# Kernel tuning notes

Hardware: AMD Instinct MI355X
Metric: run time of the kernel (lower is better)

The kernel has to match this reference:

```python
import jax, jax.numpy as jnp
import numpy as np

C = 1024      # num_classes (leaves of a balanced binary tree)
E = 10        # num_edges = tree depth (log2(C))
B = 8192      # batch size


def _build_hierarchy_buffers():
    """Replicates HierarchicalLLLoss.__init__ for a balanced binary tree.

    edges_from_leaf[i][j] is leaf i's ancestor edge j levels up (j=0 is the
    leaf's own edge). Its leaf set is all leaves sharing the top (E-j) bits,
    i.e. l >> j == i >> j.
    """
    i = np.arange(C)
    onehot_num = np.zeros((C, C, E), dtype=np.float32)
    onehot_den = np.zeros((C, C, E), dtype=np.float32)
    for j in range(E):
        onehot_num[:, :, j] = ((i[:, None] >> j) == (i[None, :] >> j))
    for j in range(E - 1):
        # den column j uses the ancestor one level higher (edges_from_leaf[i][1:])
        onehot_den[:, :, j] = ((i[:, None] >> (j + 1)) == (i[None, :] >> (j + 1)))
    onehot_den[:, :, E - 1] = 1.0  # root: all leaves
    # per-edge weights: exponential decay with level (leaf edge heaviest)
    w = np.exp(-0.5 * np.arange(E, dtype=np.float32))
    weights = np.broadcast_to(w, (C, E)).copy()
    return (jnp.asarray(onehot_num), jnp.asarray(onehot_den), jnp.asarray(weights))


def setup_inputs() -> dict:
    key = jax.random.key(0)
    k1, k2 = jax.random.split(key)
    # inputs are softmax-style probabilities (strictly positive)
    logits = jax.random.uniform(k1, (B, C), dtype=jnp.float32, minval=0.0, maxval=1.0)
    inputs = logits / jnp.sum(logits, axis=1, keepdims=True)
    target = jax.random.randint(k2, (B,), 0, C, dtype=jnp.int64 if jax.config.read('jax_enable_x64') else jnp.int32)
    onehot_num, onehot_den, weights = _build_hierarchy_buffers()
    return {"inputs": inputs, "target": target,
            "onehot_num": onehot_num, "onehot_den": onehot_den,
            "weights": weights}


def reference(inputs, target, onehot_num, onehot_den, weights):
    # gather per-sample onehot slabs: [B, C, E]
    oh_num = onehot_num[target]
    oh_den = onehot_den[target]
    # bmm(inputs[B,1,C], oh[B,C,E]) -> [B, E]
    num = jnp.einsum('bc,bce->be', inputs, oh_num)
    den = jnp.einsum('bc,bce->be', inputs, oh_den)
    idx = num != 0
    safe_num = jnp.where(idx, num, 1.0)
    safe_den = jnp.where(idx, den, 1.0)
    terms = jnp.where(idx, -jnp.log(safe_num / safe_den), num)
    per_sample = jnp.sum(jnp.flip(weights[target] * terms, axis=1), axis=1)
    return jnp.mean(per_sample)
```

## Files before the change

### kernel.cpp

```cpp
#include <hip/hip_runtime.h>

#define C_CLASSES 1024
#define E_EDGES   10
#define BATCH     8192
#define WPB       4
#define NBLOCKS   (BATCH / WPB)

__device__ __constant__ const float WLN2[E_EDGES] = {
    0.69314718f, 0.42041501f, 0.25499462f, 0.15466204f, 0.09380727f,
    0.05689699f, 0.03450977f, 0.02093123f, 0.01269543f, 0.00770017f};

__global__ __launch_bounds__(256) void hll_main(const float* __restrict__ in,
                                                const int*   __restrict__ tgt,
                                                float* __restrict__ loss) {
    const int tid  = threadIdx.x;
    const int lane = tid & 63;
    const int wave = tid >> 6;
    const int b    = blockIdx.x * WPB + wave;

    const int t = tgt[b];
    const float* row = in + (size_t)b * C_CLASSES + lane * 16;
    const float4 a0 = ((const float4*)row)[0];
    const float4 a1 = ((const float4*)row)[1];
    const float4 a2 = ((const float4*)row)[2];
    const float4 a3 = ((const float4*)row)[3];

    const float p0 = a0.x + a0.y, p1 = a0.z + a0.w;
    const float p2 = a1.x + a1.y, p3 = a1.z + a1.w;
    const float p4 = a2.x + a2.y, p5 = a2.z + a2.w;
    const float p6 = a3.x + a3.y, p7 = a3.z + a3.w;
    const float q0 = p0 + p1, q1 = p2 + p3;
    const float q2 = p4 + p5, q3 = p6 + p7;
    const float r0 = q0 + q1, r1 = q2 + q3;
    float T = r0 + r1;

    const float s4 = T;
    T += __shfl_xor(T, 1);  const float s5  = T;
    T += __shfl_xor(T, 2);  const float s6  = T;
    T += __shfl_xor(T, 4);  const float s7  = T;
    T += __shfl_xor(T, 8);  const float s8  = T;
    T += __shfl_xor(T, 16); const float s9  = T;
    T += __shfl_xor(T, 32); const float s10 = T;

    if (lane == (t >> 4)) {
        const int ti = t & 15;
        const float s3 = (ti & 8) ? r1 : r0;
        const float s2 = (ti & 8) ? ((ti & 4) ? q3 : q2)
                                  : ((ti & 4) ? q1 : q0);
        const float s1 = (ti & 8) ? ((ti & 4) ? ((ti & 2) ? p7 : p6)
                                              : ((ti & 2) ? p5 : p4))
                                  : ((ti & 4) ? ((ti & 2) ? p3 : p2)
                                              : ((ti & 2) ? p1 : p0));
        const float s0 =
            (ti & 8) ? ((ti & 4) ? ((ti & 2) ? ((ti & 1) ? a3.w : a3.z)
                                             : ((ti & 1) ? a3.y : a3.x))
                                 : ((ti & 2) ? ((ti & 1) ? a2.w : a2.z)
                                             : ((ti & 1) ? a2.y : a2.x)))
                     : ((ti & 4) ? ((ti & 2) ? ((ti & 1) ? a1.w : a1.z)
                                             : ((ti & 1) ? a1.y : a1.x))
                                 : ((ti & 2) ? ((ti & 1) ? a0.w : a0.z)
                                             : ((ti & 1) ? a0.y : a0.x)));

        const float sv[11] = {s0, s1, s2, s3, s4, s5, s6, s7, s8, s9, s10};
        float ls[11];
        #pragma unroll
        for (int j = 0; j < 11; ++j) ls[j] = __log2f(sv[j]);

        float sum = 0.0f;
        #pragma unroll
        for (int j = 0; j < E_EDGES; ++j) {
            const float term = (sv[j] != 0.0f) ? (ls[j + 1] - ls[j]) : 0.0f;
            sum += WLN2[j] * term;
        }
        loss[b] = sum;
    }
}

__global__ __launch_bounds__(256) void hll_reduce(const float* __restrict__ loss,
                                                  float* __restrict__ out) {
    const int tid = threadIdx.x;
    const float4* l4 = (const float4*)loss;
    float v = 0.0f;
    #pragma unroll
    for (int k = 0; k < BATCH / (256 * 4); ++k) {
        const float4 q = l4[tid + k * 256];
        v += (q.x + q.y) + (q.z + q.w);
    }

    v += __shfl_xor(v, 1);
    v += __shfl_xor(v, 2);
    v += __shfl_xor(v, 4);
    v += __shfl_xor(v, 8);
    v += __shfl_xor(v, 16);
    v += __shfl_xor(v, 32);

    __shared__ float ws[4];
    const int wave = tid >> 6, lane = tid & 63;
    if (lane == 0) ws[wave] = v;
    __syncthreads();
    if (tid == 0)
        out[0] = ((ws[0] + ws[1]) + (ws[2] + ws[3])) * (1.0f / (float)BATCH);
}

extern "C" void kernel_launch(void* const* d_in, const int* in_sizes, int n_in,
                              void* d_out, int out_size, void* d_ws, size_t ws_size,
                              hipStream_t stream) {
    const float* in  = (const float*)d_in[0];
    const int*   tgt = (const int*)d_in[1];
    float* loss = (float*)d_ws;

    hll_main<<<NBLOCKS, 256, 0, stream>>>(in, tgt, loss);
    hll_reduce<<<1, 256, 0, stream>>>(loss, (float*)d_out);
}
```

Before: 11.68 us.

## Fuse per-sample loss and batch mean into one kernel via last-block reduction

```diff
diff --git a/kernel.cpp b/kernel.cpp
--- a/kernel.cpp
+++ b/kernel.cpp
@@ -3,16 +3,18 @@
 #define C_CLASSES 1024
 #define E_EDGES   10
 #define BATCH     8192
-#define WPB       4
+#define WPB       16
 #define NBLOCKS   (BATCH / WPB)
 
 __device__ __constant__ const float WLN2[E_EDGES] = {
     0.69314718f, 0.42041501f, 0.25499462f, 0.15466204f, 0.09380727f,
     0.05689699f, 0.03450977f, 0.02093123f, 0.01269543f, 0.00770017f};
 
-__global__ __launch_bounds__(256) void hll_main(const float* __restrict__ in,
-                                                const int*   __restrict__ tgt,
-                                                float* __restrict__ loss) {
+__global__ __launch_bounds__(1024) void hll_fused(const float* __restrict__ in,
+                                                  const int*   __restrict__ tgt,
+                                                  float* __restrict__ partial,
+                                                  unsigned int* __restrict__ counter,
+                                                  float* __restrict__ out) {
     const int tid  = threadIdx.x;
     const int lane = tid & 63;
     const int wave = tid >> 6;
@@ -41,6 +43,9 @@
     T += __shfl_xor(T, 8);  const float s8  = T;
     T += __shfl_xor(T, 16); const float s9  = T;
     T += __shfl_xor(T, 32); const float s10 = T;
+
+    __shared__ float wsum[WPB];
+    __shared__ int   lastf;
 
     if (lane == (t >> 4)) {
         const int ti = t & 15;
@@ -72,34 +77,43 @@
             const float term = (sv[j] != 0.0f) ? (ls[j + 1] - ls[j]) : 0.0f;
             sum += WLN2[j] * term;
         }
-        loss[b] = sum;
-    }
-}
-
-__global__ __launch_bounds__(256) void hll_reduce(const float* __restrict__ loss,
-                                                  float* __restrict__ out) {
-    const int tid = threadIdx.x;
-    const float4* l4 = (const float4*)loss;
-    float v = 0.0f;
-    #pragma unroll
-    for (int k = 0; k < BATCH / (256 * 4); ++k) {
-        const float4 q = l4[tid + k * 256];
-        v += (q.x + q.y) + (q.z + q.w);
+        wsum[wave] = sum;
     }
 
-    v += __shfl_xor(v, 1);
-    v += __shfl_xor(v, 2);
-    v += __shfl_xor(v, 4);
-    v += __shfl_xor(v, 8);
-    v += __shfl_xor(v, 16);
-    v += __shfl_xor(v, 32);
+    __syncthreads();
 
-    __shared__ float ws[4];
-    const int wave = tid >> 6, lane = tid & 63;
-    if (lane == 0) ws[wave] = v;
+    if (tid == 0) {
+        float bsum = 0.0f;
+        #pragma unroll
+        for (int w = 0; w < WPB; ++w) bsum += wsum[w];
+        partial[blockIdx.x] = bsum;
+        __threadfence();
+        const unsigned int old = atomicAdd(counter, 1u);
+        lastf = (((old + 1u) & (NBLOCKS - 1u)) == 0u) ? 1 : 0;
+    }
     __syncthreads();
-    if (tid == 0)
-        out[0] = ((ws[0] + ws[1]) + (ws[2] + ws[3])) * (1.0f / (float)BATCH);
+
+    if (lastf) {
+        __threadfence();
+        float v = (tid < NBLOCKS) ? atomicAdd(&partial[tid], 0.0f) : 0.0f;
+
+        v += __shfl_xor(v, 1);
+        v += __shfl_xor(v, 2);
+        v += __shfl_xor(v, 4);
+        v += __shfl_xor(v, 8);
+        v += __shfl_xor(v, 16);
+        v += __shfl_xor(v, 32);
+
+        __shared__ float fs[WPB];
+        if (lane == 0) fs[wave] = v;
+        __syncthreads();
+        if (tid == 0) {
+            float total = 0.0f;
+            #pragma unroll
+            for (int w = 0; w < WPB; ++w) total += fs[w];
+            out[0] = total * (1.0f / (float)BATCH);
+        }
+    }
 }
 
 extern "C" void kernel_launch(void* const* d_in, const int* in_sizes, int n_in,
@@ -107,8 +121,9 @@
                               hipStream_t stream) {
     const float* in  = (const float*)d_in[0];
     const int*   tgt = (const int*)d_in[1];
-    float* loss = (float*)d_ws;
+    unsigned int* counter = (unsigned int*)d_ws;
+    float* partial = (float*)((char*)d_ws + 256);
 
-    hll_main<<<NBLOCKS, 256, 0, stream>>>(in, tgt, loss);
-    hll_reduce<<<1, 256, 0, stream>>>(loss, (float*)d_out);
+    hll_fused<<<NBLOCKS, 1024, 0, stream>>>(in, tgt, partial, counter,
+                                            (float*)d_out);
 }
```

New measurement: 20.21 us. 73.0% more time.
